# Kernel optimization log

Hardware: AMD Instinct MI355X
Metric: run time of the kernel (lower is better)

The kernel has to match this reference:

```python
import jax, jax.numpy as jnp
import numpy as np

T, B, D, O, U = 64, 32768, 6, 3, 6


def setup_inputs() -> dict:
    key = jax.random.key(0)
    ks = jax.random.split(key, 8)
    measurements = jax.random.normal(ks[0], (T, B, O), dtype=jnp.float32)
    inputs_seq = jax.random.normal(ks[1], (T, B, U), dtype=jnp.float32)
    mean0 = jax.random.normal(ks[2], (B, D), dtype=jnp.float32)
    # initial covariance: 0.1 * I, positive definite
    cov0 = jnp.broadcast_to(0.1 * jnp.eye(D, dtype=jnp.float32), (B, D, D))
    # linear motion model params (jacobian = A), kept near-stable
    A = jnp.eye(D, dtype=jnp.float32) + 0.01 * jax.random.normal(ks[3], (D, D), dtype=jnp.float32)
    Bm = 0.1 * jax.random.normal(ks[4], (D, U), dtype=jnp.float32)
    Q_tril = jnp.tril(0.05 * jax.random.normal(ks[5], (D, D), dtype=jnp.float32)) + 0.1 * jnp.eye(D, dtype=jnp.float32)
    # linear measurement model params (jacobian = C)
    C = jax.random.normal(ks[6], (O, D), dtype=jnp.float32) / np.sqrt(D)
    R_tril = jnp.tril(0.05 * jax.random.normal(ks[7], (O, O), dtype=jnp.float32)) + 0.1 * jnp.eye(O, dtype=jnp.float32)
    return {"measurements": measurements, "inputs_seq": inputs_seq, "mean0": mean0,
            "cov0": cov0, "A": A, "Bm": Bm, "Q_tril": Q_tril, "C": C, "R_tril": R_tril}


def reference(measurements, inputs_seq, mean0, cov0, A, Bm, Q_tril, C, R_tril):
    Qc = Q_tril @ Q_tril.T            # (D, D) dynamics covariance
    Rc = R_tril @ R_tril.T            # (O, O) measurement covariance
    I = jnp.eye(mean0.shape[-1], dtype=mean0.dtype)

    def step(carry, xs):
        mean, cov = carry             # (B, D), (B, D, D)
        z, u = xs                     # (B, O), (B, U)
        # --- predict ---
        pred_mean = mean @ A.T + u @ Bm.T                        # (B, D)
        pred_cov = jnp.einsum('ij,bjk,lk->bil', A, cov, A) + Qc  # (B, D, D)
        # --- update ---
        pred_meas = pred_mean @ C.T                              # (B, O)
        innovation = z - pred_meas
        S = jnp.einsum('ij,bjk,lk->bil', C, pred_cov, C) + Rc    # (B, O, O)
        PCt = jnp.einsum('bij,kj->bik', pred_cov, C)             # (B, D, O)
        K = PCt @ jnp.linalg.inv(S)                              # (B, D, O)
        new_mean = pred_mean + jnp.einsum('bij,bj->bi', K, innovation)
        new_cov = (I - jnp.einsum('bij,jk->bik', K, C)) @ pred_cov
        return (new_mean, new_cov), new_mean

    (_, _), means = jax.lax.scan(step, (mean0, cov0), (measurements, inputs_seq))
    return means  # (T, B, D)
```

## Files before the change

### kernel.cpp

```cpp
#include <hip/hip_runtime.h>


#define T_STEPS 64
#define BATCH   32768
#define NCOEF   90
#define NCHUNK  8
#define CLEN    8

#define G_OFF   23040
#define GV_OFF  24192
#define WS_NEED (GV_OFF + NCHUNK * BATCH * 6 * 4)

__device__ __forceinline__ float rdlane(float v, int lane) {
    return __int_as_float(__builtin_amdgcn_readlane(__float_as_int(v), lane));
}

__global__ __launch_bounds__(64) void ekf_precompute(
    const float* __restrict__ cov0, const float* __restrict__ Ag,
    const float* __restrict__ Bg,   const float* __restrict__ Qtg,
    const float* __restrict__ Cg,   const float* __restrict__ Rtg,
    float* __restrict__ coef, float* __restrict__ Gmat, int writeG)
{
    __shared__ float sA[36], sB[36], sC[18], sQt[36], sRt[9];
    __shared__ float Qc[36], Rc[9];
    __shared__ float Mall[T_STEPS * 36];
    const int tid = threadIdx.x;

    if (tid < 36) { sA[tid] = Ag[tid]; sB[tid] = Bg[tid]; sQt[tid] = Qtg[tid]; }
    if (tid < 18) sC[tid] = Cg[tid];
    if (tid < 9)  sRt[tid] = Rtg[tid];
    __syncthreads();

    if (tid < 36) {
        int i = tid / 6, j = tid % 6; float s = 0.f;
        #pragma unroll
        for (int k = 0; k < 6; ++k) s += sQt[i*6+k] * sQt[j*6+k];
        Qc[tid] = s;
    } else if (tid < 45) {
        int q = tid - 36, i = q / 3, j = q % 3; float s = 0.f;
        #pragma unroll
        for (int k = 0; k < 3; ++k) s += sRt[i*3+k] * sRt[j*3+k];
        Rc[q] = s;
    }
    __syncthreads();

    const int i6 = tid / 6, j6 = tid % 6;
    const int i3 = tid / 3, j3 = tid % 3;
    const int qS = (tid >= 36 && tid < 45) ? tid - 36 : 0;
    const int sa = qS / 3, sb = qS % 3;

    float Ai[6], Aj[6], Acol[6], Bcol[6], Cst[18], Crow[6], Ca[6];
    float qcv = 0.f, rcv = 0.f;
    #pragma unroll
    for (int l = 0; l < 6; ++l) { Ai[l]=0.f; Aj[l]=0.f; Acol[l]=0.f; Bcol[l]=0.f; Crow[l]=0.f; Ca[l]=0.f; }
    #pragma unroll
    for (int l = 0; l < 18; ++l) Cst[l] = 0.f;

    if (tid < 36) {
        #pragma unroll
        for (int l = 0; l < 6; ++l) {
            Ai[l] = sA[i6*6+l]; Aj[l] = sA[j6*6+l];
            Acol[l] = sA[l*6+j6]; Bcol[l] = sB[l*6+j6];
        }
        #pragma unroll
        for (int l = 0; l < 18; ++l) Cst[l] = sC[l];
        qcv = Qc[tid];
    }
    if (tid < 18) {
        #pragma unroll
        for (int l = 0; l < 6; ++l) Crow[l] = sC[j3*6+l];
    }
    if (tid >= 36 && tid < 45) {
        #pragma unroll
        for (int l = 0; l < 6; ++l) Ca[l] = sC[sa*6+l];
        rcv = Rc[qS];
    }

    float Preg = 0.f;
    if (tid < 36) Preg = cov0[tid];
    __syncthreads();

    for (int t = 0; t < T_STEPS; ++t) {
        float Pf[36];
        #pragma unroll
        for (int e = 0; e < 36; ++e) Pf[e] = rdlane(Preg, e);
        float p1 = qcv;
        #pragma unroll
        for (int k = 0; k < 6; ++k) {
            float tmp = 0.f;
            #pragma unroll
            for (int l = 0; l < 6; ++l) tmp += Pf[k*6+l] * Aj[l];
            p1 += Ai[k] * tmp;
        }

        float p1r[6];
        #pragma unroll
        for (int l = 0; l < 6; ++l) p1r[l] = __shfl(p1, i3*6 + l);
        float pct = p1r[0]*Crow[0] + p1r[1]*Crow[1] + p1r[2]*Crow[2]
                  + p1r[3]*Crow[3] + p1r[4]*Crow[4] + p1r[5]*Crow[5];

        float sv = rcv;
        #pragma unroll
        for (int l = 0; l < 6; ++l) sv += Ca[l] * __shfl(pct, l*3 + sb);

        float a  = rdlane(sv, 36), b  = rdlane(sv, 37), c  = rdlane(sv, 38);
        float d  = rdlane(sv, 39), e  = rdlane(sv, 40), f  = rdlane(sv, 41);
        float g  = rdlane(sv, 42), h  = rdlane(sv, 43), i9 = rdlane(sv, 44);
        float idet = 1.0f / (a*(e*i9-f*h) - b*(d*i9-f*g) + c*(d*h-e*g));
        float s0 =  (e*i9-f*h)*idet, s1 = -(b*i9-c*h)*idet, s2 =  (b*f-c*e)*idet;
        float s3 = -(d*i9-f*g)*idet, s4 =  (a*i9-c*g)*idet, s5 = -(a*f-c*d)*idet;
        float s6 =  (d*h-e*g)*idet,  s7 = -(a*h-b*g)*idet,  s8 =  (a*e-b*d)*idet;

        float Pi0 = __shfl(pct, i6*3 + 0);
        float Pi1 = __shfl(pct, i6*3 + 1);
        float Pi2 = __shfl(pct, i6*3 + 2);
        float K0 = Pi0*s0 + Pi1*s3 + Pi2*s6;
        float K1 = Pi0*s1 + Pi1*s4 + Pi2*s7;
        float K2 = Pi0*s2 + Pi1*s5 + Pi2*s8;

        float ik[6];
        #pragma unroll
        for (int k = 0; k < 6; ++k)
            ik[k] = ((i6 == k) ? 1.f : 0.f)
                  - (K0*Cst[0*6+k] + K1*Cst[1*6+k] + K2*Cst[2*6+k]);

        float p1col[6];
        #pragma unroll
        for (int k = 0; k < 6; ++k) p1col[k] = __shfl(p1, k*6 + j6);

        float mo = 0.f, no = 0.f, pn = 0.f;
        #pragma unroll
        for (int k = 0; k < 6; ++k) {
            mo += ik[k] * Acol[k];
            no += ik[k] * Bcol[k];
            pn += ik[k] * p1col[k];
        }

        if (tid < 36) {
            coef[t*NCOEF + tid]      = mo;
            coef[t*NCOEF + 36 + tid] = no;
            if (j6 < 3)
                coef[t*NCOEF + 72 + i6*3 + j6] = (j6 == 0 ? K0 : (j6 == 1 ? K1 : K2));
            Mall[t*36 + tid] = mo;
        }
        Preg = pn;
    }
    __syncthreads();

    if (writeG) {
        const int im = (tid < 36) ? i6 : 0;
        for (int cch = 0; cch < NCHUNK; ++cch) {
            float Gv = (tid < 36) ? Mall[(cch*CLEN)*36 + tid] : 0.f;
            for (int s = 1; s < CLEN; ++s) {
                float acc = 0.f;
                #pragma unroll
                for (int k = 0; k < 6; ++k) {
                    float gk = __shfl(Gv, k*6 + j6);
                    acc += Mall[(cch*CLEN + s)*36 + im*6 + k] * gk;
                }
                Gv = acc;
            }
            if (tid < 36) Gmat[cch*36 + tid] = Gv;
        }
    }
}

__global__ __launch_bounds__(256) void ekf_gpass(
    const float* __restrict__ z, const float* __restrict__ u,
    const float* __restrict__ coef, float* __restrict__ g)
{
    const int c = blockIdx.y;
    const int b = blockIdx.x * 256 + threadIdx.x;

    float m[6] = {0.f, 0.f, 0.f, 0.f, 0.f, 0.f};

    #pragma unroll
    for (int s = 0; s < CLEN; ++s) {
        const int t = c * CLEN + s;
        const float* cf = coef + t * NCOEF;
        const int base  = t * BATCH + b;

        const float*  zp = z + (size_t)base * 3;
        const float2* up = (const float2*)(u + (size_t)base * 6);
        float zz[3] = { zp[0], zp[1], zp[2] };
        float2 u01 = up[0], u23 = up[1], u45 = up[2];
        float uu[6] = { u01.x, u01.y, u23.x, u23.y, u45.x, u45.y };

        float nm[6];
        #pragma unroll
        for (int i = 0; i < 6; ++i) {
            float s2 = 0.f;
            #pragma unroll
            for (int j = 0; j < 6; ++j) s2 += cf[i*6+j] * m[j];
            #pragma unroll
            for (int j = 0; j < 6; ++j) s2 += cf[36 + i*6 + j] * uu[j];
            #pragma unroll
            for (int j = 0; j < 3; ++j) s2 += cf[72 + i*3 + j] * zz[j];
            nm[i] = s2;
        }
        #pragma unroll
        for (int i = 0; i < 6; ++i) m[i] = nm[i];
    }

    float2* gp = (float2*)(g + ((size_t)c * BATCH + b) * 6);
    gp[0] = make_float2(m[0], m[1]);
    gp[1] = make_float2(m[2], m[3]);
    gp[2] = make_float2(m[4], m[5]);
}

__global__ __launch_bounds__(256) void ekf_opass(
    const float* __restrict__ z, const float* __restrict__ u,
    const float* __restrict__ mean0, const float* __restrict__ coef,
    const float* __restrict__ Gmat, const float* __restrict__ g,
    float* __restrict__ out)
{
    const int c = blockIdx.y;
    const int b = blockIdx.x * 256 + threadIdx.x;

    float m[6];
    {
        const float2* mp = (const float2*)(mean0 + (size_t)b * 6);
        float2 a0 = mp[0], a1 = mp[1], a2 = mp[2];
        m[0]=a0.x; m[1]=a0.y; m[2]=a1.x; m[3]=a1.y; m[4]=a2.x; m[5]=a2.y;
    }

    for (int cc = 0; cc < c; ++cc) {
        const float* G = Gmat + cc * 36;
        const float2* gp = (const float2*)(g + ((size_t)cc * BATCH + b) * 6);
        float2 g01 = gp[0], g23 = gp[1], g45 = gp[2];
        float gv[6] = { g01.x, g01.y, g23.x, g23.y, g45.x, g45.y };
        float nm[6];
        #pragma unroll
        for (int i = 0; i < 6; ++i) {
            float s2 = gv[i];
            #pragma unroll
            for (int j = 0; j < 6; ++j) s2 += G[i*6+j] * m[j];
            nm[i] = s2;
        }
        #pragma unroll
        for (int i = 0; i < 6; ++i) m[i] = nm[i];
    }

    #pragma unroll
    for (int s = 0; s < CLEN; ++s) {
        const int t = c * CLEN + s;
        const float* cf = coef + t * NCOEF;
        const int base  = t * BATCH + b;

        const float*  zp = z + (size_t)base * 3;
        const float2* up = (const float2*)(u + (size_t)base * 6);
        float zz[3] = { zp[0], zp[1], zp[2] };
        float2 u01 = up[0], u23 = up[1], u45 = up[2];
        float uu[6] = { u01.x, u01.y, u23.x, u23.y, u45.x, u45.y };

        float nm[6];
        #pragma unroll
        for (int i = 0; i < 6; ++i) {
            float s2 = 0.f;
            #pragma unroll
            for (int j = 0; j < 6; ++j) s2 += cf[i*6+j] * m[j];
            #pragma unroll
            for (int j = 0; j < 6; ++j) s2 += cf[36 + i*6 + j] * uu[j];
            #pragma unroll
            for (int j = 0; j < 3; ++j) s2 += cf[72 + i*3 + j] * zz[j];
            nm[i] = s2;
        }

        float2* op = (float2*)(out + (size_t)base * 6);
        op[0] = make_float2(nm[0], nm[1]);
        op[1] = make_float2(nm[2], nm[3]);
        op[2] = make_float2(nm[4], nm[5]);

        #pragma unroll
        for (int i = 0; i < 6; ++i) m[i] = nm[i];
    }
}

__global__ __launch_bounds__(128) void ekf_mean(
    const float* __restrict__ z, const float* __restrict__ u,
    const float* __restrict__ mean0, const float* __restrict__ coef,
    float* __restrict__ out)
{
    __shared__ float sc[T_STEPS * NCOEF];
    const int tid = threadIdx.x;
    for (int idx = tid; idx < T_STEPS * NCOEF; idx += 128) sc[idx] = coef[idx];

    const int b = blockIdx.x * 128 + tid;
    float m[6];
    {
        const float2* mp = (const float2*)(mean0 + b * 6);
        float2 a0 = mp[0], a1 = mp[1], a2 = mp[2];
        m[0]=a0.x; m[1]=a0.y; m[2]=a1.x; m[3]=a1.y; m[4]=a2.x; m[5]=a2.y;
    }
    __syncthreads();

    #pragma unroll 2
    for (int t = 0; t < T_STEPS; ++t) {
        const float* cf  = &sc[t * NCOEF];
        const int base   = t * BATCH + b;
        const float*  zp = z + base * 3;
        const float2* up = (const float2*)(u + (size_t)base * 6);

        float zz[3] = { zp[0], zp[1], zp[2] };
        float2 u01 = up[0], u23 = up[1], u45 = up[2];
        float uu[6] = { u01.x, u01.y, u23.x, u23.y, u45.x, u45.y };

        float nm[6];
        #pragma unroll
        for (int i = 0; i < 6; ++i) {
            float s = 0.f;
            #pragma unroll
            for (int j = 0; j < 6; ++j) s += cf[i*6+j] * m[j];
            #pragma unroll
            for (int j = 0; j < 6; ++j) s += cf[36 + i*6 + j] * uu[j];
            #pragma unroll
            for (int j = 0; j < 3; ++j) s += cf[72 + i*3 + j] * zz[j];
            nm[i] = s;
        }

        float2* op = (float2*)(out + (size_t)base * 6);
        op[0] = make_float2(nm[0], nm[1]);
        op[1] = make_float2(nm[2], nm[3]);
        op[2] = make_float2(nm[4], nm[5]);

        #pragma unroll
        for (int i = 0; i < 6; ++i) m[i] = nm[i];
    }
}

extern "C" void kernel_launch(void* const* d_in, const int* in_sizes, int n_in,
                              void* d_out, int out_size, void* d_ws, size_t ws_size,
                              hipStream_t stream) {
    const float* meas  = (const float*)d_in[0];
    const float* useq  = (const float*)d_in[1];
    const float* mean0 = (const float*)d_in[2];
    const float* cov0  = (const float*)d_in[3];
    const float* A     = (const float*)d_in[4];
    const float* Bm    = (const float*)d_in[5];
    const float* Qt    = (const float*)d_in[6];
    const float* C     = (const float*)d_in[7];
    const float* Rt    = (const float*)d_in[8];
    float* out  = (float*)d_out;

    float* coef = (float*)d_ws;
    float* Gmat = (float*)((char*)d_ws + G_OFF);
    float* gvec = (float*)((char*)d_ws + GV_OFF);

    const bool scan_path = (ws_size >= (size_t)WS_NEED);

    ekf_precompute<<<1, 64, 0, stream>>>(cov0, A, Bm, Qt, C, Rt, coef, Gmat,
                                         scan_path ? 1 : 0);
    if (scan_path) {
        dim3 grid(BATCH / 256, NCHUNK);
        ekf_gpass<<<grid, 256, 0, stream>>>(meas, useq, coef, gvec);
        ekf_opass<<<grid, 256, 0, stream>>>(meas, useq, mean0, coef, Gmat, gvec, out);
    } else {
        ekf_mean<<<BATCH / 128, 128, 0, stream>>>(meas, useq, mean0, coef, out);
    }
}
```

Before: 190.5 us.

## Fuse chunk g-pass and output pass into one kernel with LDS exchange

Merges the two chunked-scan kernels into one kernel. Each 512-thread block gives one wavefront per time chunk for 64 batch lanes, and the per-chunk partial means are exchanged through shared memory instead of a global workspace. The z and u inputs for a chunk are loaded once and kept in registers for both passes, so the second read of the inputs, the global g round trip and one kernel launch go away. Shuffles in the precompute kernel are also hoisted and grouped. In exchange the kernel needs more registers for the cached inputs and a block-wide barrier, which may lower occupancy.

```diff
diff --git a/kernel.cpp b/kernel.cpp
--- a/kernel.cpp
+++ b/kernel.cpp
@@ -8,8 +8,7 @@
 #define CLEN    8
 
 #define G_OFF   23040
-#define GV_OFF  24192
-#define WS_NEED (GV_OFF + NCHUNK * BATCH * 6 * 4)
+#define WS_NEED (G_OFF + 1152)
 
 __device__ __forceinline__ float rdlane(float v, int lane) {
     return __int_as_float(__builtin_amdgcn_readlane(__float_as_int(v), lane));
@@ -93,15 +92,25 @@
             p1 += Ai[k] * tmp;
         }
 
-        float p1r[6];
-        #pragma unroll
-        for (int l = 0; l < 6; ++l) p1r[l] = __shfl(p1, i3*6 + l);
+        float p1r[6], p1col[6];
+        #pragma unroll
+        for (int l = 0; l < 6; ++l) p1r[l]   = __shfl(p1, i3*6 + l);
+        #pragma unroll
+        for (int k = 0; k < 6; ++k) p1col[k] = __shfl(p1, k*6 + j6);
+
         float pct = p1r[0]*Crow[0] + p1r[1]*Crow[1] + p1r[2]*Crow[2]
                   + p1r[3]*Crow[3] + p1r[4]*Crow[4] + p1r[5]*Crow[5];
 
+        float pcol[6], Pi0, Pi1, Pi2;
+        #pragma unroll
+        for (int l = 0; l < 6; ++l) pcol[l] = __shfl(pct, l*3 + sb);
+        Pi0 = __shfl(pct, i6*3 + 0);
+        Pi1 = __shfl(pct, i6*3 + 1);
+        Pi2 = __shfl(pct, i6*3 + 2);
+
         float sv = rcv;
         #pragma unroll
-        for (int l = 0; l < 6; ++l) sv += Ca[l] * __shfl(pct, l*3 + sb);
+        for (int l = 0; l < 6; ++l) sv += Ca[l] * pcol[l];
 
         float a  = rdlane(sv, 36), b  = rdlane(sv, 37), c  = rdlane(sv, 38);
         float d  = rdlane(sv, 39), e  = rdlane(sv, 40), f  = rdlane(sv, 41);
@@ -111,9 +120,6 @@
         float s3 = -(d*i9-f*g)*idet, s4 =  (a*i9-c*g)*idet, s5 = -(a*f-c*d)*idet;
         float s6 =  (d*h-e*g)*idet,  s7 = -(a*h-b*g)*idet,  s8 =  (a*e-b*d)*idet;
 
-        float Pi0 = __shfl(pct, i6*3 + 0);
-        float Pi1 = __shfl(pct, i6*3 + 1);
-        float Pi2 = __shfl(pct, i6*3 + 2);
         float K0 = Pi0*s0 + Pi1*s3 + Pi2*s6;
         float K1 = Pi0*s1 + Pi1*s4 + Pi2*s7;
         float K2 = Pi0*s2 + Pi1*s5 + Pi2*s8;
@@ -123,10 +129,6 @@
         for (int k = 0; k < 6; ++k)
             ik[k] = ((i6 == k) ? 1.f : 0.f)
                   - (K0*Cst[0*6+k] + K1*Cst[1*6+k] + K2*Cst[2*6+k]);
-
-        float p1col[6];
-        #pragma unroll
-        for (int k = 0; k < 6; ++k) p1col[k] = __shfl(p1, k*6 + j6);
 
         float mo = 0.f, no = 0.f, pn = 0.f;
         #pragma unroll
@@ -152,12 +154,13 @@
         for (int cch = 0; cch < NCHUNK; ++cch) {
             float Gv = (tid < 36) ? Mall[(cch*CLEN)*36 + tid] : 0.f;
             for (int s = 1; s < CLEN; ++s) {
+                float gk[6];
+                #pragma unroll
+                for (int k = 0; k < 6; ++k) gk[k] = __shfl(Gv, k*6 + j6);
                 float acc = 0.f;
                 #pragma unroll
-                for (int k = 0; k < 6; ++k) {
-                    float gk = __shfl(Gv, k*6 + j6);
-                    acc += Mall[(cch*CLEN + s)*36 + im*6 + k] * gk;
-                }
+                for (int k = 0; k < 6; ++k)
+                    acc += Mall[(cch*CLEN + s)*36 + im*6 + k] * gk[k];
                 Gv = acc;
             }
             if (tid < 36) Gmat[cch*36 + tid] = Gv;
@@ -165,13 +168,17 @@
     }
 }
 
-__global__ __launch_bounds__(256) void ekf_gpass(
+__global__ __launch_bounds__(512) void ekf_scan(
     const float* __restrict__ z, const float* __restrict__ u,
-    const float* __restrict__ coef, float* __restrict__ g)
+    const float* __restrict__ mean0, const float* __restrict__ coef,
+    const float* __restrict__ Gmat, float* __restrict__ out)
 {
-    const int c = blockIdx.y;
-    const int b = blockIdx.x * 256 + threadIdx.x;
-
+    __shared__ float gl[NCHUNK][64][6];
+    const int lane = threadIdx.x & 63;
+    const int c    = __builtin_amdgcn_readfirstlane(threadIdx.x >> 6);
+    const int b    = blockIdx.x * 64 + lane;
+
+    float zz[CLEN][3], uu[CLEN][6];
     float m[6] = {0.f, 0.f, 0.f, 0.f, 0.f, 0.f};
 
     #pragma unroll
@@ -182,9 +189,10 @@
 
         const float*  zp = z + (size_t)base * 3;
         const float2* up = (const float2*)(u + (size_t)base * 6);
-        float zz[3] = { zp[0], zp[1], zp[2] };
+        zz[s][0] = zp[0]; zz[s][1] = zp[1]; zz[s][2] = zp[2];
         float2 u01 = up[0], u23 = up[1], u45 = up[2];
-        float uu[6] = { u01.x, u01.y, u23.x, u23.y, u45.x, u45.y };
+        uu[s][0]=u01.x; uu[s][1]=u01.y; uu[s][2]=u23.x;
+        uu[s][3]=u23.y; uu[s][4]=u45.x; uu[s][5]=u45.y;
 
         float nm[6];
         #pragma unroll
@@ -193,52 +201,40 @@
             #pragma unroll
             for (int j = 0; j < 6; ++j) s2 += cf[i*6+j] * m[j];
             #pragma unroll
-            for (int j = 0; j < 6; ++j) s2 += cf[36 + i*6 + j] * uu[j];
-            #pragma unroll
-            for (int j = 0; j < 3; ++j) s2 += cf[72 + i*3 + j] * zz[j];
+            for (int j = 0; j < 6; ++j) s2 += cf[36 + i*6 + j] * uu[s][j];
+            #pragma unroll
+            for (int j = 0; j < 3; ++j) s2 += cf[72 + i*3 + j] * zz[s][j];
             nm[i] = s2;
         }
         #pragma unroll
         for (int i = 0; i < 6; ++i) m[i] = nm[i];
     }
 
-    float2* gp = (float2*)(g + ((size_t)c * BATCH + b) * 6);
-    gp[0] = make_float2(m[0], m[1]);
-    gp[1] = make_float2(m[2], m[3]);
-    gp[2] = make_float2(m[4], m[5]);
-}
-
-__global__ __launch_bounds__(256) void ekf_opass(
-    const float* __restrict__ z, const float* __restrict__ u,
-    const float* __restrict__ mean0, const float* __restrict__ coef,
-    const float* __restrict__ Gmat, const float* __restrict__ g,
-    float* __restrict__ out)
-{
-    const int c = blockIdx.y;
-    const int b = blockIdx.x * 256 + threadIdx.x;
-
-    float m[6];
+    #pragma unroll
+    for (int i = 0; i < 6; ++i) gl[c][lane][i] = m[i];
+    __syncthreads();
+
+    float bm[6];
     {
         const float2* mp = (const float2*)(mean0 + (size_t)b * 6);
         float2 a0 = mp[0], a1 = mp[1], a2 = mp[2];
-        m[0]=a0.x; m[1]=a0.y; m[2]=a1.x; m[3]=a1.y; m[4]=a2.x; m[5]=a2.y;
-    }
-
+        bm[0]=a0.x; bm[1]=a0.y; bm[2]=a1.x; bm[3]=a1.y; bm[4]=a2.x; bm[5]=a2.y;
+    }
     for (int cc = 0; cc < c; ++cc) {
         const float* G = Gmat + cc * 36;
-        const float2* gp = (const float2*)(g + ((size_t)cc * BATCH + b) * 6);
-        float2 g01 = gp[0], g23 = gp[1], g45 = gp[2];
-        float gv[6] = { g01.x, g01.y, g23.x, g23.y, g45.x, g45.y };
+        float gv[6];
+        #pragma unroll
+        for (int i = 0; i < 6; ++i) gv[i] = gl[cc][lane][i];
         float nm[6];
         #pragma unroll
         for (int i = 0; i < 6; ++i) {
             float s2 = gv[i];
             #pragma unroll
-            for (int j = 0; j < 6; ++j) s2 += G[i*6+j] * m[j];
+            for (int j = 0; j < 6; ++j) s2 += G[i*6+j] * bm[j];
             nm[i] = s2;
         }
         #pragma unroll
-        for (int i = 0; i < 6; ++i) m[i] = nm[i];
+        for (int i = 0; i < 6; ++i) bm[i] = nm[i];
     }
 
     #pragma unroll
@@ -247,22 +243,16 @@
         const float* cf = coef + t * NCOEF;
         const int base  = t * BATCH + b;
 
-        const float*  zp = z + (size_t)base * 3;
-        const float2* up = (const float2*)(u + (size_t)base * 6);
-        float zz[3] = { zp[0], zp[1], zp[2] };
-        float2 u01 = up[0], u23 = up[1], u45 = up[2];
-        float uu[6] = { u01.x, u01.y, u23.x, u23.y, u45.x, u45.y };
-
         float nm[6];
         #pragma unroll
         for (int i = 0; i < 6; ++i) {
             float s2 = 0.f;
             #pragma unroll
-            for (int j = 0; j < 6; ++j) s2 += cf[i*6+j] * m[j];
-            #pragma unroll
-            for (int j = 0; j < 6; ++j) s2 += cf[36 + i*6 + j] * uu[j];
-            #pragma unroll
-            for (int j = 0; j < 3; ++j) s2 += cf[72 + i*3 + j] * zz[j];
+            for (int j = 0; j < 6; ++j) s2 += cf[i*6+j] * bm[j];
+            #pragma unroll
+            for (int j = 0; j < 6; ++j) s2 += cf[36 + i*6 + j] * uu[s][j];
+            #pragma unroll
+            for (int j = 0; j < 3; ++j) s2 += cf[72 + i*3 + j] * zz[s][j];
             nm[i] = s2;
         }
 
@@ -272,7 +262,7 @@
         op[2] = make_float2(nm[4], nm[5]);
 
         #pragma unroll
-        for (int i = 0; i < 6; ++i) m[i] = nm[i];
+        for (int i = 0; i < 6; ++i) bm[i] = nm[i];
     }
 }
 
@@ -301,9 +291,9 @@
         const float*  zp = z + base * 3;
         const float2* up = (const float2*)(u + (size_t)base * 6);
 
-        float zz[3] = { zp[0], zp[1], zp[2] };
+        float zzv[3] = { zp[0], zp[1], zp[2] };
         float2 u01 = up[0], u23 = up[1], u45 = up[2];
-        float uu[6] = { u01.x, u01.y, u23.x, u23.y, u45.x, u45.y };
+        float uuv[6] = { u01.x, u01.y, u23.x, u23.y, u45.x, u45.y };
 
         float nm[6];
         #pragma unroll
@@ -312,9 +302,9 @@
             #pragma unroll
             for (int j = 0; j < 6; ++j) s += cf[i*6+j] * m[j];
             #pragma unroll
-            for (int j = 0; j < 6; ++j) s += cf[36 + i*6 + j] * uu[j];
-            #pragma unroll
-            for (int j = 0; j < 3; ++j) s += cf[72 + i*3 + j] * zz[j];
+            for (int j = 0; j < 6; ++j) s += cf[36 + i*6 + j] * uuv[j];
+            #pragma unroll
+            for (int j = 0; j < 3; ++j) s += cf[72 + i*3 + j] * zzv[j];
             nm[i] = s;
         }
 
@@ -344,16 +334,13 @@
 
     float* coef = (float*)d_ws;
     float* Gmat = (float*)((char*)d_ws + G_OFF);
-    float* gvec = (float*)((char*)d_ws + GV_OFF);
 
     const bool scan_path = (ws_size >= (size_t)WS_NEED);
 
     ekf_precompute<<<1, 64, 0, stream>>>(cov0, A, Bm, Qt, C, Rt, coef, Gmat,
                                          scan_path ? 1 : 0);
     if (scan_path) {
-        dim3 grid(BATCH / 256, NCHUNK);
-        ekf_gpass<<<grid, 256, 0, stream>>>(meas, useq, coef, gvec);
-        ekf_opass<<<grid, 256, 0, stream>>>(meas, useq, mean0, coef, Gmat, gvec, out);
+        ekf_scan<<<BATCH / 64, 512, 0, stream>>>(meas, useq, mean0, coef, Gmat, out);
     } else {
         ekf_mean<<<BATCH / 128, 128, 0, stream>>>(meas, useq, mean0, coef, out);
     }
```

Result: slower. 198.5 us (+4.2%).
